# Kernel tuning notes

Hardware: AMD Instinct MI355X
Metric: run time of the kernel (lower is better)

The kernel has to match this reference:

```python
import jax, jax.numpy as jnp
import numpy as np

EPS = 1e-5


def spectral_conv3d(x, w):
    # x: [B, C, X, Y, Z] real; w: [4, Cin, Cout, m1, m2, m3, 2] (4 frequency corners, real/imag)
    m1, m2, m3 = w.shape[3], w.shape[4], w.shape[5]
    wc = w[..., 0] + 1j * w[..., 1]
    X, Y, Z = x.shape[-3], x.shape[-2], x.shape[-1]
    xf = jnp.fft.rfftn(x, axes=(-3, -2, -1), norm="ortho")  # [B,C,X,Y,Z//2+1] complex
    mul = lambda a, b: jnp.einsum('bixyz,ioxyz->boxyz', a, b)
    out = jnp.zeros(xf.shape, dtype=xf.dtype)
    out = out.at[:, :, :m1, :m2, :m3].set(mul(xf[:, :, :m1, :m2, :m3], wc[0]))
    out = out.at[:, :, -m1:, :m2, :m3].set(mul(xf[:, :, -m1:, :m2, :m3], wc[1]))
    out = out.at[:, :, :m1, -m2:, :m3].set(mul(xf[:, :, :m1, -m2:, :m3], wc[2]))
    out = out.at[:, :, -m1:, -m2:, :m3].set(mul(xf[:, :, -m1:, -m2:, :m3], wc[3]))
    return jnp.fft.irfftn(out, s=(X, Y, Z), axes=(-3, -2, -1), norm="ortho")


def batchnorm3d(x, g, b):
    # training-mode BatchNorm3d: stats over (B, X, Y, Z) per channel, biased variance
    mean = jnp.mean(x, axis=(0, 2, 3, 4), keepdims=True)
    var = jnp.var(x, axis=(0, 2, 3, 4), keepdims=True)
    xhat = (x - mean) * jax.lax.rsqrt(var + EPS)
    return xhat * g[None, :, None, None, None] + b[None, :, None, None, None]


def setup_inputs() -> dict:
    key = jax.random.key(0)
    ks = jax.random.split(key, 12)
    B, X, Y, Z = 4, 64, 64, 64
    W, M = 32, 8
    scale = 1.0 / (W * W)
    return {
        "x": jax.random.normal(ks[0], (B, X, Y, Z, 3), dtype=jnp.float32),
        "fc0_w": jax.random.normal(ks[1], (W, 3), dtype=jnp.float32) * 0.3,
        "fc0_b": jax.random.normal(ks[2], (W,), dtype=jnp.float32) * 0.1,
        "sw": scale * jax.random.uniform(ks[3], (4, 4, W, W, M, M, M, 2), dtype=jnp.float32),
        "cw": jax.random.normal(ks[4], (4, W, W), dtype=jnp.float32) * (1.0 / np.sqrt(W)),
        "cb": jax.random.normal(ks[5], (4, W), dtype=jnp.float32) * 0.05,
        "gamma": jnp.ones((4, W), dtype=jnp.float32),
        "beta": jnp.zeros((4, W), dtype=jnp.float32),
        "fc1_w": jax.random.normal(ks[6], (128, W), dtype=jnp.float32) * (1.0 / np.sqrt(W)),
        "fc1_b": jax.random.normal(ks[7], (128,), dtype=jnp.float32) * 0.05,
        "fc2_w": jax.random.normal(ks[8], (1, 128), dtype=jnp.float32) * (1.0 / np.sqrt(128.0)),
        "fc2_b": jax.random.normal(ks[9], (1,), dtype=jnp.float32) * 0.05,
    }


def reference(x, fc0_w, fc0_b, sw, cw, cb, gamma, beta, fc1_w, fc1_b, fc2_w, fc2_b):
    # lift: [B,X,Y,Z,3] -> [B,X,Y,Z,W] -> [B,W,X,Y,Z]
    h = jnp.einsum('bxyzi,wi->bxyzw', x, fc0_w) + fc0_b
    h = jnp.transpose(h, (0, 4, 1, 2, 3))
    for i in range(4):
        x1 = spectral_conv3d(h, sw[i])
        x2 = jnp.einsum('bcxyz,oc->boxyz', h, cw[i]) + cb[i][None, :, None, None, None]
        h = batchnorm3d(x1 + x2, gamma[i], beta[i])
        if i < 3:
            h = jax.nn.relu(h)
    h = jnp.transpose(h, (0, 2, 3, 4, 1))  # [B,X,Y,Z,W]
    h = jax.nn.relu(jnp.einsum('bxyzw,fw->bxyzf', h, fc1_w) + fc1_b)
    out = jnp.einsum('bxyzf,of->bxyzo', h, fc2_w) + fc2_b
    return out
```

## Files before the change

### kernel.cpp

```cpp
#include <hip/hip_runtime.h>

#define TW_STEP 0.09817477042468103f

typedef __bf16 bf16x8 __attribute__((ext_vector_type(8)));
typedef __bf16 bf16x4 __attribute__((ext_vector_type(4)));
typedef __bf16 bf16x2 __attribute__((ext_vector_type(2)));
typedef float  f32x4  __attribute__((ext_vector_type(4)));

static constexpr size_t SZ_P   = (size_t)4*32*64*64*64*2;
static constexpr size_t SZ_A   = (size_t)4*32*8*64*64*8;
static constexpr size_t SZ_B2  = (size_t)4*32*8*16*64*8;
static constexpr size_t SZ_XF  = (size_t)4*32*8*16*16*8;
static constexpr size_t OFF_P  = 0;
static constexpr size_t OFF_A  = OFF_P + SZ_P;
static constexpr size_t OFF_B2 = OFF_A + SZ_A;
static constexpr size_t OFF_XF = OFF_B2 + SZ_B2;
static constexpr size_t OFF_YF = OFF_XF + SZ_XF;
static constexpr size_t OFF_TW  = OFF_YF + SZ_XF;
static constexpr size_t OFF_BNP = OFF_TW + 512;
static constexpr size_t OFF_W1B = OFF_BNP + 1024;
static constexpr size_t OFF_B1P = OFF_W1B + 8192;
static constexpr size_t OFF_WFZ = OFF_B1P + 512;
static constexpr size_t OFF_WZ  = OFF_WFZ + 4096;
static constexpr size_t OFF_WY  = OFF_WZ + 8192;


__global__ void k_twinit(float2* tw, __bf16* wfz, __bf16* wz, __bf16* wy) {
    int t = threadIdx.x;
    if (t < 64) { float s, c; sincosf(TW_STEP * t, &s, &c); tw[t] = make_float2(c, s); }
    for (int e = t; e < 1024; e += 256) {
        int half = e >> 9, rem = e & 511, kg = rem >> 7, tt = (rem >> 3) & 15, j = e & 7;
        int z = half * 32 + kg * 8 + j, k = tt >> 1;
        float ang = TW_STEP * (float)((k * z) & 63);
        float val = (tt & 1) ? -sinf(ang) : cosf(ang);
        __bf16 hi = (__bf16)val;
        wfz[e] = hi;
        wfz[1024 + e] = (__bf16)(val - (float)hi);
    }
    for (int e = t; e < 2048; e += 256) {
        int z = e >> 5, tt = e & 31, k = tt >> 1;
        float ang = TW_STEP * (float)((k * z) & 63);
        float val;
        if (tt == 0) val = 1.f;
        else if (tt == 1) val = 0.f;
        else val = (tt & 1) ? (-2.f * sinf(ang)) : (2.f * cosf(ang));
        __bf16 hi = (__bf16)val;
        wz[e] = hi;
        wz[2048 + e] = (__bf16)(val - (float)hi);
    }
    for (int e = t; e < 4096; e += 256) {
        int j = e & 7, l = (e >> 3) & 63, hl = (e >> 9) & 1, nt = (e >> 10) & 1, kc = (e >> 11) & 1;
        int f = l & 15;
        int F = f < 8 ? f : f + 48;
        int y = kc * 32 + ((l >> 4) & 3) * 8 + j;
        float ang = TW_STEP * (float)((F * y) & 63);
        float val = nt ? sinf(ang) : cosf(ang);
        __bf16 hi = (__bf16)val;
        wy[e] = hl ? (__bf16)(val - (float)hi) : hi;
    }
}

__global__ __launch_bounds__(256) void k_lift(const float* __restrict__ x,
                                              const float* __restrict__ w,
                                              const float* __restrict__ bias,
                                              __bf16* __restrict__ P) {
    int v = blockIdx.x * 256 + threadIdx.x;
    int z = v & 63, y = (v >> 6) & 63, xx = (v >> 12) & 63, b = v >> 18;
    float i0 = x[(size_t)v * 3 + 0], i1 = x[(size_t)v * 3 + 1], i2 = x[(size_t)v * 3 + 2];
#pragma unroll
    for (int c = 0; c < 32; c++) {
        float val = bias[c] + w[c * 3 + 0] * i0 + w[c * 3 + 1] * i1 + w[c * 3 + 2] * i2;
        P[(size_t)(((b * 32 + c) * 64 + xx) * 64 + y) * 64 + z] = (__bf16)val;
    }
}

__global__ __launch_bounds__(256) void k_zfwd(const __bf16* __restrict__ P,
                                              const __bf16* __restrict__ wfz,
                                              const float* __restrict__ bnp, int relu,
                                              __bf16* __restrict__ T1b) {
    int blk = blockIdx.x;
    int x = blk & 63, c = (blk >> 6) & 31, b = blk >> 11;
    __shared__ __bf16 hs2[64][72];
    __shared__ float ttmp[16][66];
    int tid = threadIdx.x, l = tid & 63, w = tid >> 6;
    {
        int y = tid >> 2, q = tid & 3;
        float scb = 1.f, shb = 0.f;
        if (bnp) { scb = bnp[c]; shb = bnp[32 + c]; }
        const __bf16* src = P + ((size_t)((b * 32 + c) * 64 + x) * 64 + y) * 64 + q * 16;
        bf16x8 v0 = ((const bf16x8*)src)[0], v1 = ((const bf16x8*)src)[1];
        bf16x8 o0, o1;
#pragma unroll
        for (int j = 0; j < 8; j++) {
            float a = (float)v0[j], bb = (float)v1[j];
            if (bnp) {
                a = fmaf(a, scb, shb); bb = fmaf(bb, scb, shb);
                if (relu) { a = fmaxf(a, 0.f); bb = fmaxf(bb, 0.f); }
            }
            o0[j] = (__bf16)a; o1[j] = (__bf16)bb;
        }
        *(bf16x8*)&hs2[y][q * 16] = o0;
        *(bf16x8*)&hs2[y][q * 16 + 8] = o1;
    }
    __syncthreads();
    int col = l & 15, kg = l >> 4;
    f32x4 acc = (f32x4){0.f, 0.f, 0.f, 0.f};
#pragma unroll
    for (int half = 0; half < 2; half++) {
        bf16x8 a = *(const bf16x8*)&hs2[w * 16 + col][half * 32 + kg * 8];
        const __bf16* wp = wfz + ((half * 4 + kg) * 16 + col) * 8;
        bf16x8 bh = *(const bf16x8*)wp;
        bf16x8 blo = *(const bf16x8*)(wp + 1024);
        acc = __builtin_amdgcn_mfma_f32_16x16x32_bf16(a, bh, acc, 0, 0, 0);
        acc = __builtin_amdgcn_mfma_f32_16x16x32_bf16(a, blo, acc, 0, 0, 0);
    }
#pragma unroll
    for (int r = 0; r < 4; r++) ttmp[col][w * 16 + kg * 4 + r] = acc[r];
    __syncthreads();
    if (tid < 128) {
        int k = tid >> 4, y0 = (tid & 15) * 4;
        float4 re4 = *(const float4*)&ttmp[2 * k][y0];
        float4 im4 = *(const float4*)&ttmp[2 * k + 1][y0];
        bf16x8 outv;
        outv[0] = (__bf16)re4.x; outv[1] = (__bf16)im4.x;
        outv[2] = (__bf16)re4.y; outv[3] = (__bf16)im4.y;
        outv[4] = (__bf16)re4.z; outv[5] = (__bf16)im4.z;
        outv[6] = (__bf16)re4.w; outv[7] = (__bf16)im4.w;
        size_t ob = (size_t)((b * 32 + c) * 8 + k) * 4096 + x * 64 + y0;
        *(bf16x8*)(T1b + ob * 2) = outv;
    }
}

__global__ __launch_bounds__(256) void k_dftm(const __bf16* __restrict__ in,
                                              __bf16* __restrict__ outb,
                                              float2* __restrict__ outf,
                                              const __bf16* __restrict__ wy,
                                              int mode) {
    int rb = blockIdx.x * 16;
    __shared__ __bf16 af[32 * 72];
    __shared__ float dd[2][2][16][18];
    int tid = threadIdx.x, l = tid & 63, w = tid >> 6;
    {
        int r = tid >> 4, yq = tid & 15;
        bf16x8 v = *(const bf16x8*)(in + ((size_t)(rb + r) * 64 + yq * 4) * 2);
        bf16x4 re, im;
#pragma unroll
        for (int j = 0; j < 4; j++) { re[j] = v[2 * j]; im[j] = v[2 * j + 1]; }
        *(bf16x4*)&af[(2 * r) * 72 + yq * 4] = re;
        *(bf16x4*)&af[(2 * r + 1) * 72 + yq * 4] = im;
    }
    __syncthreads();
    int mt = w >> 1, nt = w & 1, col = l & 15, kg = l >> 4;
    f32x4 acc = (f32x4){0.f, 0.f, 0.f, 0.f};
#pragma unroll
    for (int kc = 0; kc < 2; kc++) {
        bf16x8 a = *(const bf16x8*)&af[(mt * 16 + col) * 72 + kc * 32 + kg * 8];
        const __bf16* wp = wy + (kc * 2 + nt) * 1024 + l * 8;
        bf16x8 bh = *(const bf16x8*)wp;
        bf16x8 blo = *(const bf16x8*)(wp + 512);
        acc = __builtin_amdgcn_mfma_f32_16x16x32_bf16(a, bh, acc, 0, 0, 0);
        acc = __builtin_amdgcn_mfma_f32_16x16x32_bf16(a, blo, acc, 0, 0, 0);
    }
#pragma unroll
    for (int r = 0; r < 4; r++) dd[mt][nt][kg * 4 + r][col] = acc[r];
    __syncthreads();
    {
        int cr = tid >> 4, f = tid & 15;
        int mt2 = cr >> 3, tre = (2 * cr) & 15, tim = (2 * cr + 1) & 15;
        float Re = dd[mt2][0][tre][f] + dd[mt2][1][tim][f];
        float Im = dd[mt2][0][tim][f] - dd[mt2][1][tre][f];
        int rg = rb + cr;
        if (mode == 0) {
            union { __bf16 h[2]; unsigned u; } pk;
            pk.h[0] = (__bf16)Re; pk.h[1] = (__bf16)Im;
            ((unsigned*)outb)[(rg >> 6) * 1024 + f * 64 + (rg & 63)] = pk.u;
        } else {
            outf[rg * 16 + f] = make_float2(Re, Im);
        }
    }
}

__global__ __launch_bounds__(128) void k_specmul(const float2* __restrict__ Xf,
                                                 const float* __restrict__ swl,
                                                 float2* __restrict__ Yf) {
    int m = blockIdx.x;
    int kxi = m & 15, kyi = (m >> 4) & 15, kz = m >> 8;
    int corner = (kxi >= 8 ? 1 : 0) + (kyi >= 8 ? 2 : 0);
    int mx = kxi & 7, my = kyi & 7;
    __shared__ float2 wsd[1024];
    __shared__ float2 xfs[128];
    int tid = threadIdx.x;
    const float* wb = swl + (size_t)corner * 1048576 + mx * 128 + my * 16 + kz * 2;
    for (int idx = tid; idx < 1024; idx += 128) {
        int i = idx >> 5, o = idx & 31;
        const float* p = wb + (size_t)i * 32768 + o * 1024;
        wsd[idx] = make_float2(p[0], p[1]);
    }
    {
        int b = tid >> 5, i = tid & 31;
        xfs[tid] = Xf[(((b * 32 + i) * 8 + kz) * 16 + kyi) * 16 + kxi];
    }
    __syncthreads();
    int b = tid >> 5, o = tid & 31;
    float ar = 0.f, ai = 0.f;
#pragma unroll
    for (int i = 0; i < 32; i++) {
        float2 xv = xfs[b * 32 + i];
        float2 wv = wsd[i * 32 + o];
        ar += xv.x * wv.x - xv.y * wv.y;
        ai += xv.x * wv.y + xv.y * wv.x;
    }
    const float s = 1.0f / 262144.0f;
    Yf[(((b * 32 + o) * 8 + kz) * 16 + kyi) * 16 + kxi] = make_float2(ar * s, ai * s);
}

__global__ __launch_bounds__(256) void k_xinv(const float2* __restrict__ Yf,
                                              unsigned* __restrict__ U1p) {
    int blk = blockIdx.x;
    int kz = blk & 7, o = (blk >> 3) & 31, b = blk >> 8;
    __shared__ float2 yfs[16][17];
    __shared__ float2 tw[64];
    int tid = threadIdx.x;
    if (tid < 64) { float s, c; sincosf(TW_STEP * tid, &s, &c); tw[tid] = make_float2(c, s); }
    {
        int kyi = tid >> 4, kxi = tid & 15;
        yfs[kyi][kxi] = Yf[(size_t)((b * 32 + o) * 8 + kz) * 256 + tid];
    }
    __syncthreads();
    size_t base = (size_t)((b * 8 + kz) * 64) * 512 + o;
#pragma unroll
    for (int r = 0; r < 4; r++) {
        int idx = tid + r * 256;
        int x = idx >> 4, kyi = idx & 15;
        float ar = 0.f, ai = 0.f;
#pragma unroll
        for (int kxi = 0; kxi < 16; kxi++) {
            int f = kxi < 8 ? kxi : kxi + 48;
            float2 t = tw[(f * x) & 63];
            float2 v = yfs[kyi][kxi];
            ar += v.x * t.x - v.y * t.y;
            ai += v.x * t.y + v.y * t.x;
        }
        union { __bf16 h[2]; unsigned u; } pk;
        pk.h[0] = (__bf16)ar; pk.h[1] = (__bf16)ai;
        U1p[base + (size_t)x * 512 + kyi * 32] = pk.u;
    }
}

__global__ __launch_bounds__(256) void k_fuse(__bf16* __restrict__ P,
                                              const unsigned* __restrict__ U1p,
                                              const float* __restrict__ cwl,
                                              const float* __restrict__ cbl,
                                              const __bf16* __restrict__ wz,
                                              const float* __restrict__ bnp, int relu,
                                              float* __restrict__ part) {
    int blk = blockIdx.x;
    int yt = blk >> 8, bxi = blk & 255;
    int b = bxi >> 6, x = bxi & 63;
    int y0 = yt * 4;
    __shared__ __bf16 hs[256 * 40];
    __shared__ __bf16 u2b[4][32][20];
    __shared__ float2 twl[64];
    __shared__ float sredS[4][32], sredQ[4][32];
    int tid = threadIdx.x;
    int l = tid & 63, w = tid >> 6;
    if (tid < 64) { float s, c; sincosf(TW_STEP * tid, &s, &c); twl[tid] = make_float2(c, s); }
    __syncthreads();

    int col = l & 15, kg = l >> 4;
    bf16x8 cwf[2];
    float cbv[2];
#pragma unroll
    for (int nt = 0; nt < 2; nt++) {
        int o = nt * 16 + col;
        const float4* p4 = (const float4*)(cwl + o * 32 + kg * 8);
        float4 q0 = p4[0], q1 = p4[1];
        cwf[nt][0] = (__bf16)q0.x; cwf[nt][1] = (__bf16)q0.y;
        cwf[nt][2] = (__bf16)q0.z; cwf[nt][3] = (__bf16)q0.w;
        cwf[nt][4] = (__bf16)q1.x; cwf[nt][5] = (__bf16)q1.y;
        cwf[nt][6] = (__bf16)q1.z; cwf[nt][7] = (__bf16)q1.w;
        cbv[nt] = cbl[o];
    }

    {
        int c = tid >> 3, j = tid & 7;
        float scb = 1.f, shb = 0.f;
        if (bnp) { scb = bnp[c]; shb = bnp[32 + c]; }
        const __bf16* src = P + ((size_t)((b * 32 + c) * 64 + x) * 64 + y0) * 64 + j * 8;
#pragma unroll
        for (int q = 0; q < 4; q++) {
            bf16x8 v8 = *(const bf16x8*)(src + q * 64);
            float fv[8];
#pragma unroll
            for (int jj = 0; jj < 8; jj++) {
                float v = (float)v8[jj];
                if (bnp) { v = fmaf(v, scb, shb); if (relu) v = fmaxf(v, 0.f); }
                fv[jj] = v;
            }
#pragma unroll
            for (int s = 0; s < 8; s++) {
                int jr = (s + j) & 7;
                hs[(q * 64 + j * 8 + jr) * 40 + c] = (__bf16)fv[jr];
            }
        }
    }
    {
        int o = tid & 31, kz = tid >> 5;
        const unsigned* u1p = U1p + (size_t)((b * 8 + kz) * 64 + x) * 512 + o;
        float ur[16], ui[16];
#pragma unroll
        for (int kyi = 0; kyi < 16; kyi++) {
            union { unsigned u; __bf16 h[2]; } pk;
            pk.u = u1p[kyi * 32];
            ur[kyi] = (float)pk.h[0]; ui[kyi] = (float)pk.h[1];
        }
        float spr[8], sdr[8], spi[8], sdi[8];
#pragma unroll
        for (int p = 1; p < 8; p++) {
            spr[p] = ur[p] + ur[16 - p]; sdr[p] = ur[p] - ur[16 - p];
            spi[p] = ui[p] + ui[16 - p]; sdi[p] = ui[p] - ui[16 - p];
        }
#pragma unroll
        for (int yy = 0; yy < 4; yy++) {
            int y = y0 + yy;
            float arv = ur[0], aiv = ui[0];
            float2 t8 = twl[(8 * y) & 63];
            arv = fmaf(ur[8], t8.x, arv); arv = fmaf(ui[8], t8.y, arv);
            aiv = fmaf(ui[8], t8.x, aiv); aiv = fmaf(-ur[8], t8.y, aiv);
#pragma unroll
            for (int p = 1; p < 8; p++) {
                float2 t = twl[(p * y) & 63];
                arv = fmaf(spr[p], t.x, arv); arv = fmaf(-sdi[p], t.y, arv);
                aiv = fmaf(spi[p], t.x, aiv); aiv = fmaf(sdr[p], t.y, aiv);
            }
            union { __bf16 h[2]; unsigned u; } pk;
            pk.h[0] = (__bf16)arv; pk.h[1] = (__bf16)aiv;
            *(unsigned*)&u2b[yy][o][2 * kz] = pk.u;
        }
    }
    __syncthreads();

    f32x4 acc[4][2];
#pragma unroll
    for (int i = 0; i < 4; i++) {
        bf16x8 a = *(const bf16x8*)&hs[((w * 4 + i) * 16 + col) * 40 + kg * 8];
#pragma unroll
        for (int nt = 0; nt < 2; nt++) {
            acc[i][nt] = (f32x4){0.f, 0.f, 0.f, 0.f};
            acc[i][nt] = __builtin_amdgcn_mfma_f32_16x16x32_bf16(a, cwf[nt], acc[i][nt], 0, 0, 0);
        }
    }
    {
        bf16x8 u2f[2];
#pragma unroll
        for (int nt = 0; nt < 2; nt++) {
            bf16x8 v = (bf16x8){(__bf16)0.f, (__bf16)0.f, (__bf16)0.f, (__bf16)0.f,
                                (__bf16)0.f, (__bf16)0.f, (__bf16)0.f, (__bf16)0.f};
            if (kg < 2) {
                bf16x4 lo = *(const bf16x4*)&u2b[w][nt * 16 + col][kg * 8];
                bf16x4 hi = *(const bf16x4*)&u2b[w][nt * 16 + col][kg * 8 + 4];
                v[0] = lo[0]; v[1] = lo[1]; v[2] = lo[2]; v[3] = lo[3];
                v[4] = hi[0]; v[5] = hi[1]; v[6] = hi[2]; v[7] = hi[3];
            }
            u2f[nt] = v;
        }
#pragma unroll
        for (int i = 0; i < 4; i++) {
            int z = i * 16 + col;
            const __bf16* wp = wz + z * 32 + kg * 8;
            bf16x8 wzh = *(const bf16x8*)wp;
            bf16x8 wzl = *(const bf16x8*)(wp + 2048);
#pragma unroll
            for (int nt = 0; nt < 2; nt++) {
                acc[i][nt] = __builtin_amdgcn_mfma_f32_16x16x32_bf16(wzh, u2f[nt], acc[i][nt], 0, 0, 0);
                acc[i][nt] = __builtin_amdgcn_mfma_f32_16x16x32_bf16(wzl, u2f[nt], acc[i][nt], 0, 0, 0);
            }
        }
    }

    float sacc[2] = {0.f, 0.f}, ssacc[2] = {0.f, 0.f};
#pragma unroll
    for (int nt = 0; nt < 2; nt++) {
        int o = nt * 16 + col;
        __bf16* dstb = P + ((size_t)((b * 32 + o) * 64 + x) * 64 + (y0 + w)) * 64;
#pragma unroll
        for (int i = 0; i < 4; i++) {
            int z0s = i * 16 + kg * 4;
            bf16x4 outv;
#pragma unroll
            for (int r = 0; r < 4; r++) {
                float f = acc[i][nt][r] + cbv[nt];
                sacc[nt] += f;
                ssacc[nt] = fmaf(f, f, ssacc[nt]);
                outv[r] = (__bf16)f;
            }
            *(bf16x4*)(dstb + z0s) = outv;
        }
    }
#pragma unroll
    for (int nt = 0; nt < 2; nt++) {
        sacc[nt] += __shfl_xor(sacc[nt], 16, 64);
        sacc[nt] += __shfl_xor(sacc[nt], 32, 64);
        ssacc[nt] += __shfl_xor(ssacc[nt], 16, 64);
        ssacc[nt] += __shfl_xor(ssacc[nt], 32, 64);
    }
    if (l < 16) {
        sredS[w][col] = sacc[0]; sredS[w][16 + col] = sacc[1];
        sredQ[w][col] = ssacc[0]; sredQ[w][16 + col] = ssacc[1];
    }
    __syncthreads();
    if (tid < 32) {
        float S = sredS[0][tid] + sredS[1][tid] + sredS[2][tid] + sredS[3][tid];
        float SS = sredQ[0][tid] + sredQ[1][tid] + sredQ[2][tid] + sredQ[3][tid];
        part[((size_t)tid * 4096 + blk) * 2 + 0] = S;
        part[((size_t)tid * 4096 + blk) * 2 + 1] = SS;
    }
}

__global__ __launch_bounds__(256) void k_red2(const float* __restrict__ part,
                                              const float* __restrict__ gamma,
                                              const float* __restrict__ beta,
                                              float* __restrict__ bnp) {
    int c = blockIdx.x;
    int tid = threadIdx.x;
    const float2* pc = (const float2*)(part + (size_t)c * 8192);
    float s = 0.f, ss = 0.f;
#pragma unroll
    for (int q = 0; q < 16; q++) { float2 v = pc[tid * 16 + q]; s += v.x; ss += v.y; }
#pragma unroll
    for (int d = 32; d; d >>= 1) { s += __shfl_down(s, d, 64); ss += __shfl_down(ss, d, 64); }
    __shared__ float ws[8];
    if ((tid & 63) == 0) { ws[(tid >> 6) * 2] = s; ws[(tid >> 6) * 2 + 1] = ss; }
    __syncthreads();
    if (tid == 0) {
        double S = (double)ws[0] + ws[2] + ws[4] + ws[6];
        double SS = (double)ws[1] + ws[3] + ws[5] + ws[7];
        const double invN = 1.0 / 1048576.0;
        double mean = S * invN;
        double var = SS * invN - mean * mean;
        float scl = gamma[c] * rsqrtf((float)var + 1e-5f);
        bnp[c] = scl;
        bnp[32 + c] = beta[c] - (float)mean * scl;
    }
}

__global__ void k_prep(const float* __restrict__ w1, const float* __restrict__ b1,
                       const float* __restrict__ bnp,
                       __bf16* __restrict__ w1b, float* __restrict__ b1p) {
    int f = threadIdx.x;
    if (f >= 128) return;
    float acc = b1[f];
#pragma unroll
    for (int c = 0; c < 32; c++) {
        float wv = w1[f * 32 + c];
        w1b[f * 32 + c] = (__bf16)(wv * bnp[c]);
        acc = fmaf(wv, bnp[32 + c], acc);
    }
    b1p[f] = acc;
}

__global__ __launch_bounds__(256) void k_head(const __bf16* __restrict__ P,
                                              const __bf16* __restrict__ w1b,
                                              const float* __restrict__ b1p,
                                              const float* __restrict__ w2,
                                              const float* __restrict__ b2,
                                              float* __restrict__ out) {
    __shared__ __bf16 hs[64 * 40];
    int tid = threadIdx.x;
    int b = blockIdx.x >> 9;
    int r0 = (blockIdx.x & 511) * 512;
    int l = tid & 63;
    int w = tid >> 6;
    int col = l & 15, kg = l >> 4, hi = l >> 4;

    bf16x8 afr[8];
    f32x4 b1q[8], w2q[8];
    {
#pragma unroll
        for (int nt = 0; nt < 8; nt++) {
            afr[nt] = *(const bf16x8*)(w1b + (nt * 16 + col) * 32 + kg * 8);
            b1q[nt] = ((const f32x4*)b1p)[nt * 4 + hi];
            w2q[nt] = ((const f32x4*)w2)[nt * 4 + hi];
        }
    }
    float b2v = b2[0];
    int sc_c = tid & 31, sc_j = tid >> 5;
    const __bf16* srcb = P + (size_t)(b * 32 + sc_c) * 262144 + r0 + sc_j * 8;

    for (int t = 0; t < 8; t++) {
        {
            bf16x8 v8 = *(const bf16x8*)(srcb + t * 64);
#pragma unroll
            for (int s = 0; s < 8; s++) {
                int jr = (s + sc_j * 4) & 7;
                hs[(sc_j * 8 + jr) * 40 + sc_c] = v8[jr];
            }
        }
        __syncthreads();
        bf16x8 hfr = *(const bf16x8*)&hs[(w * 16 + col) * 40 + kg * 8];
        f32x4 acc[8];
#pragma unroll
        for (int nt = 0; nt < 8; nt++) {
            acc[nt] = (f32x4){0.f, 0.f, 0.f, 0.f};
            acc[nt] = __builtin_amdgcn_mfma_f32_16x16x32_bf16(afr[nt], hfr, acc[nt], 0, 0, 0);
        }
        float s = 0.f;
#pragma unroll
        for (int nt = 0; nt < 8; nt++) {
#pragma unroll
            for (int r = 0; r < 4; r++) {
                float val = fmaxf(acc[nt][r] + b1q[nt][r], 0.f);
                s = fmaf(w2q[nt][r], val, s);
            }
        }
        s += __shfl_xor(s, 16, 64);
        s += __shfl_xor(s, 32, 64);
        if (l < 16)
            out[b * 262144 + r0 + t * 64 + w * 16 + l] = s + b2v;
        __syncthreads();
    }
}

extern "C" void kernel_launch(void* const* d_in, const int* in_sizes, int n_in,
                              void* d_out, int out_size, void* d_ws, size_t ws_size,
                              hipStream_t stream) {
    const float* x     = (const float*)d_in[0];
    const float* fc0_w = (const float*)d_in[1];
    const float* fc0_b = (const float*)d_in[2];
    const float* sw    = (const float*)d_in[3];
    const float* cw    = (const float*)d_in[4];
    const float* cb    = (const float*)d_in[5];
    const float* gamma = (const float*)d_in[6];
    const float* beta  = (const float*)d_in[7];
    const float* fc1_w = (const float*)d_in[8];
    const float* fc1_b = (const float*)d_in[9];
    const float* fc2_w = (const float*)d_in[10];
    const float* fc2_b = (const float*)d_in[11];

    char* ws = (char*)d_ws;
    __bf16* P    = (__bf16*)(ws + OFF_P);
    __bf16* T1b  = (__bf16*)(ws + OFF_A);
    __bf16* T2b  = (__bf16*)(ws + OFF_B2);
    unsigned* U1p = (unsigned*)(ws + OFF_B2);
    float2* Xf   = (float2*)(ws + OFF_XF);
    float2* Yf   = (float2*)(ws + OFF_YF);
    float*  part = (float*)(ws + OFF_XF);
    float2* gtw  = (float2*)(ws + OFF_TW);
    float*  bnp  = (float*)(ws + OFF_BNP);
    __bf16* w1b  = (__bf16*)(ws + OFF_W1B);
    float*  b1p  = (float*)(ws + OFF_B1P);
    __bf16* wfz  = (__bf16*)(ws + OFF_WFZ);
    __bf16* wz   = (__bf16*)(ws + OFF_WZ);
    __bf16* wy   = (__bf16*)(ws + OFF_WY);

    k_twinit<<<1, 256, 0, stream>>>(gtw, wfz, wz, wy);
    k_lift<<<4096, 256, 0, stream>>>(x, fc0_w, fc0_b, P);

    for (int i = 0; i < 4; i++) {
        const float* bprev = (i == 0) ? nullptr : (bnp + (i - 1) * 64);
        int relu = (i > 0) ? 1 : 0;
        k_zfwd<<<8192, 256, 0, stream>>>(P, wfz, bprev, relu, T1b);
        k_dftm<<<4096, 256, 0, stream>>>(T1b, T2b, nullptr, wy, 0);
        k_dftm<<<1024, 256, 0, stream>>>(T2b, nullptr, Xf, wy, 1);
        k_specmul<<<2048, 128, 0, stream>>>(Xf, sw + (size_t)i * 4194304, Yf);
        k_xinv<<<1024, 256, 0, stream>>>(Yf, U1p);
        k_fuse<<<4096, 256, 0, stream>>>(P, U1p, cw + i * 1024, cb + i * 32, wz, bprev, relu, part);
        k_red2<<<32, 256, 0, stream>>>(part, gamma + i * 32, beta + i * 32, bnp + i * 64);
    }

    k_prep<<<1, 128, 0, stream>>>(fc1_w, fc1_b, bnp + 3 * 64, w1b, b1p);
    k_head<<<2048, 256, 0, stream>>>(P, w1b, b1p, fc2_w, fc2_b, (float*)d_out);
}
```

Baseline: 426.6 us.

## Move y-direction inverse DFT onto MFMA and fold bias into z-DFT matmul

In the fused kernel, the scalar per-thread y inverse DFT (FMA loops over shared twiddles) becomes a bf16 MFMA product. The U1 spectrum is staged in shared memory, and a per-block y-twiddle matrix is split into hi/lo bf16 parts for accuracy. The P activation loads are issued at kernel start so their latency overlaps the spectral work, and the shared buffer is reused. The conv bias is folded into the z-DFT MFMA by adding a ones column to the wz table and a bias row to the U2 operand, which drops a per-element add. This adds an extra __syncthreads and in-kernel sincosf per block, and rounds the bias to split bf16.

```diff
diff --git a/kernel.cpp b/kernel.cpp
--- a/kernel.cpp
+++ b/kernel.cpp
@@ -43,7 +43,9 @@
         float val;
         if (tt == 0) val = 1.f;
         else if (tt == 1) val = 0.f;
-        else val = (tt & 1) ? (-2.f * sinf(ang)) : (2.f * cosf(ang));
+        else if (tt < 16) val = (tt & 1) ? (-2.f * sinf(ang)) : (2.f * cosf(ang));
+        else if (tt == 16 || tt == 17) val = 1.f;
+        else val = 0.f;
         __bf16 hi = (__bf16)val;
         wz[e] = hi;
         wz[2048 + e] = (__bf16)(val - (float)hi);
@@ -258,16 +260,21 @@
     int yt = blk >> 8, bxi = blk & 255;
     int b = bxi >> 6, x = bxi & 63;
     int y0 = yt * 4;
-    __shared__ __bf16 hs[256 * 40];
+    __shared__ __bf16 smA[256 * 40];
+    __shared__ __bf16 aY[16 * 80];
     __shared__ __bf16 u2b[4][32][20];
-    __shared__ float2 twl[64];
     __shared__ float sredS[4][32], sredQ[4][32];
     int tid = threadIdx.x;
     int l = tid & 63, w = tid >> 6;
-    if (tid < 64) { float s, c; sincosf(TW_STEP * tid, &s, &c); twl[tid] = make_float2(c, s); }
-    __syncthreads();
-
     int col = l & 15, kg = l >> 4;
+
+    int cc = tid >> 3, j0 = tid & 7;
+    const __bf16* srcP = P + (((size_t)(b * 32 + cc) * 64 + x) * 64 + y0) * 64 + j0 * 8;
+    bf16x8 pv0 = *(const bf16x8*)(srcP);
+    bf16x8 pv1 = *(const bf16x8*)(srcP + 64);
+    bf16x8 pv2 = *(const bf16x8*)(srcP + 128);
+    bf16x8 pv3 = *(const bf16x8*)(srcP + 192);
+
     bf16x8 cwf[2];
     float cbv[2];
 #pragma unroll
@@ -283,59 +290,65 @@
     }
 
     {
-        int c = tid >> 3, j = tid & 7;
+        int o = tid & 31, kz = tid >> 5;
+        const unsigned* u1p = U1p + ((size_t)(b * 8 + kz) * 64 + x) * 512 + o;
+        unsigned* rowp = (unsigned*)&smA[(kz * 32 + o) * 40];
+#pragma unroll
+        for (int kyi = 0; kyi < 16; kyi++) rowp[kyi] = u1p[kyi * 32];
+    }
+    {
+        int m = tid >> 5, kap = tid & 31;
+        int yy = m >> 1, p = m & 1, kyi = kap >> 1, q = kap & 1;
+        int F = kyi < 8 ? kyi : kyi + 48;
+        float sv, cv;
+        sincosf(TW_STEP * (float)((F * (y0 + yy)) & 63), &sv, &cv);
+        float val = (p == 0) ? (q == 0 ? cv : -sv) : (q == 0 ? sv : cv);
+        __bf16 hi = (__bf16)val;
+        aY[m * 80 + kap] = hi;
+        aY[m * 80 + 32 + kap] = (__bf16)(val - (float)hi);
+    }
+    __syncthreads();
+
+    {
+        bf16x8 ah = *(const bf16x8*)&aY[col * 80 + kg * 8];
+        bf16x8 al = *(const bf16x8*)&aY[col * 80 + 32 + kg * 8];
+#pragma unroll
+        for (int ti = 0; ti < 4; ti++) {
+            int tile = w * 4 + ti;
+            int kz = tile >> 1, oh = tile & 1;
+            bf16x8 bfv = *(const bf16x8*)&smA[(kz * 32 + oh * 16 + col) * 40 + kg * 8];
+            f32x4 d = (f32x4){0.f, 0.f, 0.f, 0.f};
+            d = __builtin_amdgcn_mfma_f32_16x16x32_bf16(ah, bfv, d, 0, 0, 0);
+            d = __builtin_amdgcn_mfma_f32_16x16x32_bf16(al, bfv, d, 0, 0, 0);
+            if (kg < 2) {
+#pragma unroll
+                for (int r = 0; r < 4; r++) {
+                    int yy = kg * 2 + (r >> 1);
+                    u2b[yy][oh * 16 + col][2 * kz + (r & 1)] = (__bf16)d[r];
+                }
+            }
+        }
+    }
+    __syncthreads();
+
+    {
         float scb = 1.f, shb = 0.f;
-        if (bnp) { scb = bnp[c]; shb = bnp[32 + c]; }
-        const __bf16* src = P + ((size_t)((b * 32 + c) * 64 + x) * 64 + y0) * 64 + j * 8;
+        if (bnp) { scb = bnp[cc]; shb = bnp[32 + cc]; }
+        bf16x8 pvs[4] = {pv0, pv1, pv2, pv3};
 #pragma unroll
         for (int q = 0; q < 4; q++) {
-            bf16x8 v8 = *(const bf16x8*)(src + q * 64);
             float fv[8];
 #pragma unroll
             for (int jj = 0; jj < 8; jj++) {
-                float v = (float)v8[jj];
+                float v = (float)pvs[q][jj];
                 if (bnp) { v = fmaf(v, scb, shb); if (relu) v = fmaxf(v, 0.f); }
                 fv[jj] = v;
             }
 #pragma unroll
             for (int s = 0; s < 8; s++) {
-                int jr = (s + j) & 7;
-                hs[(q * 64 + j * 8 + jr) * 40 + c] = (__bf16)fv[jr];
-            }
-        }
-    }
-    {
-        int o = tid & 31, kz = tid >> 5;
-        const unsigned* u1p = U1p + (size_t)((b * 8 + kz) * 64 + x) * 512 + o;
-        float ur[16], ui[16];
-#pragma unroll
-        for (int kyi = 0; kyi < 16; kyi++) {
-            union { unsigned u; __bf16 h[2]; } pk;
-            pk.u = u1p[kyi * 32];
-            ur[kyi] = (float)pk.h[0]; ui[kyi] = (float)pk.h[1];
-        }
-        float spr[8], sdr[8], spi[8], sdi[8];
-#pragma unroll
-        for (int p = 1; p < 8; p++) {
-            spr[p] = ur[p] + ur[16 - p]; sdr[p] = ur[p] - ur[16 - p];
-            spi[p] = ui[p] + ui[16 - p]; sdi[p] = ui[p] - ui[16 - p];
-        }
-#pragma unroll
-        for (int yy = 0; yy < 4; yy++) {
-            int y = y0 + yy;
-            float arv = ur[0], aiv = ui[0];
-            float2 t8 = twl[(8 * y) & 63];
-            arv = fmaf(ur[8], t8.x, arv); arv = fmaf(ui[8], t8.y, arv);
-            aiv = fmaf(ui[8], t8.x, aiv); aiv = fmaf(-ur[8], t8.y, aiv);
-#pragma unroll
-            for (int p = 1; p < 8; p++) {
-                float2 t = twl[(p * y) & 63];
-                arv = fmaf(spr[p], t.x, arv); arv = fmaf(-sdi[p], t.y, arv);
-                aiv = fmaf(spi[p], t.x, aiv); aiv = fmaf(sdr[p], t.y, aiv);
-            }
-            union { __bf16 h[2]; unsigned u; } pk;
-            pk.h[0] = (__bf16)arv; pk.h[1] = (__bf16)aiv;
-            *(unsigned*)&u2b[yy][o][2 * kz] = pk.u;
+                int jr = (s + j0) & 7;
+                smA[(q * 64 + j0 * 8 + jr) * 40 + cc] = (__bf16)fv[jr];
+            }
         }
     }
     __syncthreads();
@@ -343,7 +356,7 @@
     f32x4 acc[4][2];
 #pragma unroll
     for (int i = 0; i < 4; i++) {
-        bf16x8 a = *(const bf16x8*)&hs[((w * 4 + i) * 16 + col) * 40 + kg * 8];
+        bf16x8 a = *(const bf16x8*)&smA[((w * 4 + i) * 16 + col) * 40 + kg * 8];
 #pragma unroll
         for (int nt = 0; nt < 2; nt++) {
             acc[i][nt] = (f32x4){0.f, 0.f, 0.f, 0.f};
@@ -361,6 +374,10 @@
                 bf16x4 hi = *(const bf16x4*)&u2b[w][nt * 16 + col][kg * 8 + 4];
                 v[0] = lo[0]; v[1] = lo[1]; v[2] = lo[2]; v[3] = lo[3];
                 v[4] = hi[0]; v[5] = hi[1]; v[6] = hi[2]; v[7] = hi[3];
+            } else if (kg == 2) {
+                __bf16 ch = (__bf16)cbv[nt];
+                v[0] = ch;
+                v[1] = (__bf16)(cbv[nt] - (float)ch);
             }
             u2f[nt] = v;
         }
@@ -389,7 +406,7 @@
             bf16x4 outv;
 #pragma unroll
             for (int r = 0; r < 4; r++) {
-                float f = acc[i][nt][r] + cbv[nt];
+                float f = acc[i][nt][r];
                 sacc[nt] += f;
                 ssacc[nt] = fmaf(f, f, ssacc[nt]);
                 outv[r] = (__bf16)f;
```

New measurement: 430.4 us. No clear change (+0.9%).

## Fuse forward Y-axis partial DFT into z-DFT kernel, dropping intermediate buffer

Applied to the files above, without the earlier changes.

The z-axis truncated DFT kernel now goes on to perform the Y-axis truncated DFT for each (b,c,x) slice inside the block, using MFMA on the 16x64 intermediate held in shared memory. It writes the packed bf16 complex result straight into the buffer the X-axis DFT pass reads. This removes one kernel launch per layer and the write and read of the large T1b intermediate. In exchange each block does more work and uses extra shared memory and syncs, and the K-split sum adds a different rounding order.

```diff
diff --git a/kernel.cpp b/kernel.cpp
--- a/kernel.cpp
+++ b/kernel.cpp
@@ -74,14 +74,17 @@
     }
 }
 
-__global__ __launch_bounds__(256) void k_zfwd(const __bf16* __restrict__ P,
-                                              const __bf16* __restrict__ wfz,
-                                              const float* __restrict__ bnp, int relu,
-                                              __bf16* __restrict__ T1b) {
+__global__ __launch_bounds__(256) void k_zfwd2(const __bf16* __restrict__ P,
+                                               const __bf16* __restrict__ wfz,
+                                               const __bf16* __restrict__ wy,
+                                               const float* __restrict__ bnp, int relu,
+                                               unsigned* __restrict__ T2u) {
     int blk = blockIdx.x;
     int x = blk & 63, c = (blk >> 6) & 31, b = blk >> 11;
-    __shared__ __bf16 hs2[64][72];
+    __shared__ __bf16 hs2buf[64][72];
     __shared__ float ttmp[16][66];
+    __shared__ __bf16 af[16][72];
+    float (*ddsh)[2][16][18] = (float(*)[2][16][18])hs2buf;
     int tid = threadIdx.x, l = tid & 63, w = tid >> 6;
     {
         int y = tid >> 2, q = tid & 3;
@@ -99,43 +102,66 @@
             }
             o0[j] = (__bf16)a; o1[j] = (__bf16)bb;
         }
-        *(bf16x8*)&hs2[y][q * 16] = o0;
-        *(bf16x8*)&hs2[y][q * 16 + 8] = o1;
+        *(bf16x8*)&hs2buf[y][q * 16] = o0;
+        *(bf16x8*)&hs2buf[y][q * 16 + 8] = o1;
     }
     __syncthreads();
     int col = l & 15, kg = l >> 4;
-    f32x4 acc = (f32x4){0.f, 0.f, 0.f, 0.f};
-#pragma unroll
-    for (int half = 0; half < 2; half++) {
-        bf16x8 a = *(const bf16x8*)&hs2[w * 16 + col][half * 32 + kg * 8];
-        const __bf16* wp = wfz + ((half * 4 + kg) * 16 + col) * 8;
+    {
+        f32x4 acc = (f32x4){0.f, 0.f, 0.f, 0.f};
+#pragma unroll
+        for (int half = 0; half < 2; half++) {
+            bf16x8 a = *(const bf16x8*)&hs2buf[w * 16 + col][half * 32 + kg * 8];
+            const __bf16* wp = wfz + ((half * 4 + kg) * 16 + col) * 8;
+            bf16x8 bh = *(const bf16x8*)wp;
+            bf16x8 blo = *(const bf16x8*)(wp + 1024);
+            acc = __builtin_amdgcn_mfma_f32_16x16x32_bf16(a, bh, acc, 0, 0, 0);
+            acc = __builtin_amdgcn_mfma_f32_16x16x32_bf16(a, blo, acc, 0, 0, 0);
+        }
+#pragma unroll
+        for (int r = 0; r < 4; r++) ttmp[col][w * 16 + kg * 4 + r] = acc[r];
+    }
+    __syncthreads();
+    {
+        int row = tid >> 4, yq = tid & 15;
+        float v0 = ttmp[row][yq * 4 + 0];
+        float v1 = ttmp[row][yq * 4 + 1];
+        float v2 = ttmp[row][yq * 4 + 2];
+        float v3 = ttmp[row][yq * 4 + 3];
+        bf16x4 o;
+        o[0] = (__bf16)v0; o[1] = (__bf16)v1; o[2] = (__bf16)v2; o[3] = (__bf16)v3;
+        *(bf16x4*)&af[row][yq * 4] = o;
+    }
+    __syncthreads();
+    {
+        int nt = w & 1, kc = w >> 1;
+        bf16x8 a = *(const bf16x8*)&af[col][kc * 32 + kg * 8];
+        const __bf16* wp = wy + (kc * 2 + nt) * 1024 + l * 8;
         bf16x8 bh = *(const bf16x8*)wp;
-        bf16x8 blo = *(const bf16x8*)(wp + 1024);
-        acc = __builtin_amdgcn_mfma_f32_16x16x32_bf16(a, bh, acc, 0, 0, 0);
-        acc = __builtin_amdgcn_mfma_f32_16x16x32_bf16(a, blo, acc, 0, 0, 0);
-    }
-#pragma unroll
-    for (int r = 0; r < 4; r++) ttmp[col][w * 16 + kg * 4 + r] = acc[r];
+        bf16x8 blo = *(const bf16x8*)(wp + 512);
+        f32x4 d = (f32x4){0.f, 0.f, 0.f, 0.f};
+        d = __builtin_amdgcn_mfma_f32_16x16x32_bf16(a, bh, d, 0, 0, 0);
+        d = __builtin_amdgcn_mfma_f32_16x16x32_bf16(a, blo, d, 0, 0, 0);
+#pragma unroll
+        for (int r = 0; r < 4; r++) ddsh[kc][nt][kg * 4 + r][col] = d[r];
+    }
     __syncthreads();
     if (tid < 128) {
-        int k = tid >> 4, y0 = (tid & 15) * 4;
-        float4 re4 = *(const float4*)&ttmp[2 * k][y0];
-        float4 im4 = *(const float4*)&ttmp[2 * k + 1][y0];
-        bf16x8 outv;
-        outv[0] = (__bf16)re4.x; outv[1] = (__bf16)im4.x;
-        outv[2] = (__bf16)re4.y; outv[3] = (__bf16)im4.y;
-        outv[4] = (__bf16)re4.z; outv[5] = (__bf16)im4.z;
-        outv[6] = (__bf16)re4.w; outv[7] = (__bf16)im4.w;
-        size_t ob = (size_t)((b * 32 + c) * 8 + k) * 4096 + x * 64 + y0;
-        *(bf16x8*)(T1b + ob * 2) = outv;
+        int kz = tid >> 4, f = tid & 15;
+        int tre = 2 * kz, tim = 2 * kz + 1;
+        float Re = (ddsh[0][0][tre][f] + ddsh[1][0][tre][f])
+                 + (ddsh[0][1][tim][f] + ddsh[1][1][tim][f]);
+        float Im = (ddsh[0][0][tim][f] + ddsh[1][0][tim][f])
+                 - (ddsh[0][1][tre][f] + ddsh[1][1][tre][f]);
+        union { __bf16 h[2]; unsigned u; } pk;
+        pk.h[0] = (__bf16)Re; pk.h[1] = (__bf16)Im;
+        T2u[(size_t)((b * 32 + c) * 8 + kz) * 1024 + f * 64 + x] = pk.u;
     }
 }
 
 __global__ __launch_bounds__(256) void k_dftm(const __bf16* __restrict__ in,
-                                              __bf16* __restrict__ outb,
                                               float2* __restrict__ outf,
-                                              const __bf16* __restrict__ wy,
-                                              int mode) {
+                                              const __bf16* __restrict__ wy) {
     int rb = blockIdx.x * 16;
     __shared__ __bf16 af[32 * 72];
     __shared__ float dd[2][2][16][18];
@@ -170,13 +196,7 @@
         float Re = dd[mt2][0][tre][f] + dd[mt2][1][tim][f];
         float Im = dd[mt2][0][tim][f] - dd[mt2][1][tre][f];
         int rg = rb + cr;
-        if (mode == 0) {
-            union { __bf16 h[2]; unsigned u; } pk;
-            pk.h[0] = (__bf16)Re; pk.h[1] = (__bf16)Im;
-            ((unsigned*)outb)[(rg >> 6) * 1024 + f * 64 + (rg & 63)] = pk.u;
-        } else {
-            outf[rg * 16 + f] = make_float2(Re, Im);
-        }
+        outf[rg * 16 + f] = make_float2(Re, Im);
     }
 }
 
@@ -539,8 +559,8 @@
 
     char* ws = (char*)d_ws;
     __bf16* P    = (__bf16*)(ws + OFF_P);
-    __bf16* T1b  = (__bf16*)(ws + OFF_A);
     __bf16* T2b  = (__bf16*)(ws + OFF_B2);
+    unsigned* T2u = (unsigned*)(ws + OFF_B2);
     unsigned* U1p = (unsigned*)(ws + OFF_B2);
     float2* Xf   = (float2*)(ws + OFF_XF);
     float2* Yf   = (float2*)(ws + OFF_YF);
@@ -559,9 +579,8 @@
     for (int i = 0; i < 4; i++) {
         const float* bprev = (i == 0) ? nullptr : (bnp + (i - 1) * 64);
         int relu = (i > 0) ? 1 : 0;
-        k_zfwd<<<8192, 256, 0, stream>>>(P, wfz, bprev, relu, T1b);
-        k_dftm<<<4096, 256, 0, stream>>>(T1b, T2b, nullptr, wy, 0);
-        k_dftm<<<1024, 256, 0, stream>>>(T2b, nullptr, Xf, wy, 1);
+        k_zfwd2<<<8192, 256, 0, stream>>>(P, wfz, wy, bprev, relu, T2u);
+        k_dftm<<<1024, 256, 0, stream>>>(T2b, Xf, wy);
         k_specmul<<<2048, 128, 0, stream>>>(Xf, sw + (size_t)i * 4194304, Yf);
         k_xinv<<<1024, 256, 0, stream>>>(Yf, U1p);
         k_fuse<<<4096, 256, 0, stream>>>(P, U1p, cw + i * 1024, cb + i * 32, wz, bprev, relu, part);
```

After: 417.9 us, median of 3. 2.0% less time.
